# Kernel optimization log

Hardware: AMD Instinct MI355X
Metric: run time of the kernel (lower is better)

The kernel has to match this reference:

```python
import jax, jax.numpy as jnp
import numpy as np

B, S, D, H = 8, 1024, 768, 12
DH = D // H


def setup_inputs() -> dict:
    key = jax.random.key(0)
    ks = jax.random.split(key, 6)
    scale = 1.0 / np.sqrt(D)
    return {
        "inputs": jax.random.normal(ks[0], (B, S, D), dtype=jnp.float32),
        "Wq": jax.random.normal(ks[1], (D, D), dtype=jnp.float32) * scale,
        "bq": jnp.zeros((D,), jnp.float32),
        "Wk": jax.random.normal(ks[2], (D, D), dtype=jnp.float32) * scale,
        "bk": jnp.zeros((D,), jnp.float32),
        "Wv": jax.random.normal(ks[3], (D, D), dtype=jnp.float32) * scale,
        "bv": jnp.zeros((D,), jnp.float32),
        "Wo": jax.random.normal(ks[4], (D, D), dtype=jnp.float32) * scale,
        "bo": jnp.zeros((D,), jnp.float32),
    }


def _split_heads(x):
    # [B,S,D] -> [B,H,S,DH]
    b, s, _ = x.shape
    return x.reshape(b, s, H, DH).transpose(0, 2, 1, 3)


def reference(inputs, Wq, bq, Wk, bk, Wv, bv, Wo, bo):
    q = _split_heads(inputs @ Wq + bq)
    k = _split_heads(inputs @ Wk + bk)
    v = _split_heads(inputs @ Wv + bv)
    # scaled dot-product attention; scale = sqrt(projection_dim)
    scores = jnp.einsum("bhqd,bhkd->bhqk", q, k) / jnp.sqrt(jnp.float32(DH))
    weights = jax.nn.softmax(scores, axis=-1)
    attn = jnp.einsum("bhqk,bhkd->bhqd", weights, v)
    attn = attn.transpose(0, 2, 1, 3).reshape(inputs.shape[0], -1, D)
    return attn @ Wo + bo
```

## Files before the change

### kernel.cpp

```cpp
#include <hip/hip_runtime.h>
#include <math.h>

#define B 8
#define S 1024
#define D 768
#define H 12
#define DH 64
#define M_TOT (B * S)

typedef short bf16x8 __attribute__((ext_vector_type(8)));
typedef float f32x4 __attribute__((ext_vector_type(4)));

__device__ __forceinline__ unsigned short f2bf(float x) {
    unsigned u = __builtin_bit_cast(unsigned, x);
    u = (u + 0x7FFFu + ((u >> 16) & 1u)) >> 16;
    return (unsigned short)u;
}
__device__ __forceinline__ unsigned pk2bf(float a, float b) {
    return (unsigned)f2bf(a) | ((unsigned)f2bf(b) << 16);
}

__device__ __forceinline__ void async16(const unsigned short* g, unsigned short* l) {
    __builtin_amdgcn_global_load_lds((const __attribute__((address_space(1))) void*)g,
                                     (__attribute__((address_space(3))) void*)l, 16, 0, 0);
}

__device__ __forceinline__ void stage_tiles(const unsigned short* __restrict__ A,
                                            const unsigned short* __restrict__ Bt,
                                            unsigned short* At, unsigned short* Bs,
                                            int m0, int n0, int k0, int w, int srow, int scol) {
#pragma unroll
    for (int c = 0; c < 2; ++c) {
        const int cc = w * 2 + c;
        const int row = cc * 16 + srow;
        async16(&A[(size_t)(m0 + row) * D + k0 + scol], &At[cc * 512]);
        async16(&Bt[(size_t)(n0 + row) * D + k0 + scol], &Bs[cc * 512]);
    }
}

__global__ __launch_bounds__(256) void prep(const float* __restrict__ inputs,
                                            unsigned short* __restrict__ Abf,
                                            const float* W0, const float* W1,
                                            const float* W2, const float* W3,
                                            unsigned short* T0, unsigned short* T1,
                                            unsigned short* T2, unsigned short* T3) {
    const int bid = blockIdx.x;
    const int t = threadIdx.x;
    if (bid < 6144) {
        const int i = (bid * 256 + t) * 4;
        const float4 v = *(const float4*)&inputs[i];
        ushort4 o;
        o.x = f2bf(v.x); o.y = f2bf(v.y); o.z = f2bf(v.z); o.w = f2bf(v.w);
        *(ushort4*)&Abf[i] = o;
    } else {
        const int id = bid - 6144;
        const int z = id / 144;
        const int rem = id % 144;
        const int kx = rem % 12, ny = rem / 12;
        const float* Wsrc[4] = {W0, W1, W2, W3};
        unsigned short* Tdst[4] = {T0, T1, T2, T3};
        const float* Wm = Wsrc[z];
        unsigned short* Tm = Tdst[z];
        __shared__ float tile[64][65];
        const int r = t >> 4, c4 = (t & 15) * 4;
        const int k0 = kx * 64, n0 = ny * 64;
#pragma unroll
        for (int rr = 0; rr < 4; ++rr) {
            const float4 v = *(const float4*)&Wm[(size_t)(k0 + r + rr * 16) * D + n0 + c4];
            tile[r + rr * 16][c4 + 0] = v.x;
            tile[r + rr * 16][c4 + 1] = v.y;
            tile[r + rr * 16][c4 + 2] = v.z;
            tile[r + rr * 16][c4 + 3] = v.w;
        }
        __syncthreads();
#pragma unroll
        for (int rr = 0; rr < 4; ++rr) {
            const int nr = r + rr * 16;
            ushort4 o;
            o.x = f2bf(tile[c4 + 0][nr]);
            o.y = f2bf(tile[c4 + 1][nr]);
            o.z = f2bf(tile[c4 + 2][nr]);
            o.w = f2bf(tile[c4 + 3][nr]);
            *(ushort4*)&Tm[(size_t)(n0 + nr) * D + k0 + c4] = o;
        }
    }
}

__global__ __launch_bounds__(256) void gemm_qkv(const unsigned short* __restrict__ A,
                                                const unsigned short* __restrict__ Wtq,
                                                const unsigned short* __restrict__ Wtk,
                                                const unsigned short* __restrict__ Wtv,
                                                const float* __restrict__ bq,
                                                const float* __restrict__ bk,
                                                const float* __restrict__ bv,
                                                unsigned short* __restrict__ Qb,
                                                unsigned short* __restrict__ Kb,
                                                unsigned short* __restrict__ Vtb) {
    __shared__ unsigned short At[2][128 * 32];
    __shared__ unsigned short Bs[2][128 * 32];
    const int z = blockIdx.z;
    const unsigned short* Bt = (z == 0) ? Wtq : (z == 1) ? Wtk : Wtv;
    const float* bias = (z == 0) ? bq : (z == 1) ? bk : bv;
    const float scale = (z == 0) ? 0.125f : 1.0f;

    const int t = threadIdx.x;
    const int w = t >> 6, lane = t & 63;
    const int quad = lane >> 4, l15 = lane & 15;
    const int m0 = blockIdx.x * 128, n0 = blockIdx.y * 128;
    const int wm = (w & 1) * 64, wn = (w >> 1) * 64;
    const int srow = lane >> 2, scol = (lane & 3) * 8;

    f32x4 acc[4][4];
#pragma unroll
    for (int i = 0; i < 4; ++i)
#pragma unroll
        for (int j = 0; j < 4; ++j) acc[i][j] = (f32x4){0.f, 0.f, 0.f, 0.f};

    stage_tiles(A, Bt, At[0], Bs[0], m0, n0, 0, w, srow, scol);
    for (int kt = 0; kt < D / 32; ++kt) {
        unsigned short* Atc = At[kt & 1];
        unsigned short* Bsc = Bs[kt & 1];
        if (kt + 1 < D / 32) {
            stage_tiles(A, Bt, At[(kt + 1) & 1], Bs[(kt + 1) & 1], m0, n0, (kt + 1) * 32, w, srow, scol);
            __asm__ volatile("s_waitcnt vmcnt(4)" ::: "memory");
        } else {
            __asm__ volatile("s_waitcnt vmcnt(0)" ::: "memory");
        }
        __asm__ volatile("s_barrier" ::: "memory");
        bf16x8 af[4], bfr[4];
#pragma unroll
        for (int i = 0; i < 4; ++i)
            af[i] = *(const bf16x8*)&Atc[(wm + i * 16 + l15) * 32 + quad * 8];
#pragma unroll
        for (int j = 0; j < 4; ++j)
            bfr[j] = *(const bf16x8*)&Bsc[(wn + j * 16 + l15) * 32 + quad * 8];
#pragma unroll
        for (int i = 0; i < 4; ++i)
#pragma unroll
            for (int j = 0; j < 4; ++j)
                acc[i][j] = __builtin_amdgcn_mfma_f32_16x16x32_bf16(af[i], bfr[j], acc[i][j], 0, 0, 0);
        __asm__ volatile("s_barrier" ::: "memory");
    }

#pragma unroll
    for (int j = 0; j < 4; ++j) {
        const int col = n0 + wn + j * 16 + l15;
        const float bv2 = bias[col];
#pragma unroll
        for (int i = 0; i < 4; ++i) {
            const int row0 = m0 + wm + i * 16 + quad * 4;
            if (z < 2) {
                unsigned short* C = (z == 0) ? Qb : Kb;
#pragma unroll
                for (int r = 0; r < 4; ++r)
                    C[(size_t)(row0 + r) * D + col] = f2bf((acc[i][j][r] + bv2) * scale);
            } else {
                const int h = col >> 6, dh = col & 63;
                const int bb = row0 >> 10, s0 = row0 & 1023;
                ushort4 o;
                o.x = f2bf(acc[i][j][0] + bv2);
                o.y = f2bf(acc[i][j][1] + bv2);
                o.z = f2bf(acc[i][j][2] + bv2);
                o.w = f2bf(acc[i][j][3] + bv2);
                *(ushort4*)&Vtb[((size_t)(bb * H + h) * DH + dh) * S + s0] = o;
            }
        }
    }
}

__global__ __launch_bounds__(256) void gemm_out(const unsigned short* __restrict__ A,
                                                const unsigned short* __restrict__ Bt,
                                                const float* __restrict__ bias,
                                                float* __restrict__ C) {
    __shared__ unsigned short At[2][128 * 32];
    __shared__ unsigned short Bs[2][128 * 32];
    const int t = threadIdx.x;
    const int w = t >> 6, lane = t & 63;
    const int quad = lane >> 4, l15 = lane & 15;
    const int m0 = blockIdx.x * 128, n0 = blockIdx.y * 128;
    const int wm = (w & 1) * 64, wn = (w >> 1) * 64;
    const int srow = lane >> 2, scol = (lane & 3) * 8;

    f32x4 acc[4][4];
#pragma unroll
    for (int i = 0; i < 4; ++i)
#pragma unroll
        for (int j = 0; j < 4; ++j) acc[i][j] = (f32x4){0.f, 0.f, 0.f, 0.f};

    stage_tiles(A, Bt, At[0], Bs[0], m0, n0, 0, w, srow, scol);
    for (int kt = 0; kt < D / 32; ++kt) {
        unsigned short* Atc = At[kt & 1];
        unsigned short* Bsc = Bs[kt & 1];
        if (kt + 1 < D / 32) {
            stage_tiles(A, Bt, At[(kt + 1) & 1], Bs[(kt + 1) & 1], m0, n0, (kt + 1) * 32, w, srow, scol);
            __asm__ volatile("s_waitcnt vmcnt(4)" ::: "memory");
        } else {
            __asm__ volatile("s_waitcnt vmcnt(0)" ::: "memory");
        }
        __asm__ volatile("s_barrier" ::: "memory");
        bf16x8 af[4], bfr[4];
#pragma unroll
        for (int i = 0; i < 4; ++i)
            af[i] = *(const bf16x8*)&Atc[(wm + i * 16 + l15) * 32 + quad * 8];
#pragma unroll
        for (int j = 0; j < 4; ++j)
            bfr[j] = *(const bf16x8*)&Bsc[(wn + j * 16 + l15) * 32 + quad * 8];
#pragma unroll
        for (int i = 0; i < 4; ++i)
#pragma unroll
            for (int j = 0; j < 4; ++j)
                acc[i][j] = __builtin_amdgcn_mfma_f32_16x16x32_bf16(af[i], bfr[j], acc[i][j], 0, 0, 0);
        __asm__ volatile("s_barrier" ::: "memory");
    }

#pragma unroll
    for (int j = 0; j < 4; ++j) {
        const int col = n0 + wn + j * 16 + l15;
        const float bv = bias[col];
#pragma unroll
        for (int i = 0; i < 4; ++i) {
            const int row0 = m0 + wm + i * 16 + quad * 4;
#pragma unroll
            for (int r = 0; r < 4; ++r) C[(size_t)(row0 + r) * D + col] = acc[i][j][r] + bv;
        }
    }
}

__global__ __launch_bounds__(256) void attn_mfma(const unsigned short* __restrict__ Qg,
                                                 const unsigned short* __restrict__ Kg,
                                                 const unsigned short* __restrict__ Vtg,
                                                 unsigned short* __restrict__ ATT) {
    __shared__ unsigned short Ks[2 * 64 * 32];
    __shared__ unsigned short Vs[2 * 64 * 32];
    __shared__ unsigned short Ps2[4 * 32 * 72];

    const int t = threadIdx.x;
    const int w = t >> 6, lane = t & 63;
    const int quad = lane >> 4, l15 = lane & 15;
    const int bh = blockIdx.x % (B * H);
    const int q0 = (blockIdx.x / (B * H)) * 128;
    const int b = bh / H, h = bh % H;

    bf16x8 qb[2][2];
#pragma unroll
    for (int qh = 0; qh < 2; ++qh) {
        const size_t qoff = ((size_t)(b * S + q0 + w * 32 + qh * 16 + l15)) * D + h * DH;
        qb[qh][0] = *(const bf16x8*)&Qg[qoff + quad * 8];
        qb[qh][1] = *(const bf16x8*)&Qg[qoff + 32 + quad * 8];
    }

    f32x4 o[2][4];
#pragma unroll
    for (int qh = 0; qh < 2; ++qh)
#pragma unroll
        for (int n = 0; n < 4; ++n) o[qh][n] = (f32x4){0.f, 0.f, 0.f, 0.f};
    float m_r[2] = {-INFINITY, -INFINITY};
    float l_r[2] = {0.f, 0.f};

    const int srow = lane >> 2;
    const int scol = (((lane & 3) ^ ((lane >> 3) & 3))) * 8;
    const int fsw = ((quad ^ ((l15 >> 1) & 3)) * 8);

    unsigned short* myP = &Ps2[w * 32 * 72];

    for (int kt = 0; kt < S / 64; ++kt) {
        __syncthreads();
#pragma unroll
        for (int kc = 0; kc < 2; ++kc) {
            async16(&Kg[((size_t)(b * S + kt * 64 + w * 16 + srow)) * D + h * DH + kc * 32 + scol],
                    &Ks[kc * 2048 + w * 512]);
            async16(&Vtg[((size_t)(bh * DH + w * 16 + srow)) * S + kt * 64 + kc * 32 + scol],
                    &Vs[kc * 2048 + w * 512]);
        }
        __syncthreads();

        f32x4 sc[2][4];
#pragma unroll
        for (int n = 0; n < 4; ++n) {
            const bf16x8 ka0 = *(const bf16x8*)&Ks[0 * 2048 + (n * 16 + l15) * 32 + fsw];
            const bf16x8 ka1 = *(const bf16x8*)&Ks[1 * 2048 + (n * 16 + l15) * 32 + fsw];
#pragma unroll
            for (int qh = 0; qh < 2; ++qh) {
                f32x4 zz = (f32x4){0.f, 0.f, 0.f, 0.f};
                zz = __builtin_amdgcn_mfma_f32_16x16x32_bf16(ka0, qb[qh][0], zz, 0, 0, 0);
                zz = __builtin_amdgcn_mfma_f32_16x16x32_bf16(ka1, qb[qh][1], zz, 0, 0, 0);
                sc[qh][n] = zz;
            }
        }

        float alpha[2];
#pragma unroll
        for (int qh = 0; qh < 2; ++qh) {
            float rmax = -INFINITY;
#pragma unroll
            for (int n = 0; n < 4; ++n)
#pragma unroll
                for (int r = 0; r < 4; ++r) rmax = fmaxf(rmax, sc[qh][n][r]);
            rmax = fmaxf(rmax, __shfl_xor(rmax, 16, 64));
            rmax = fmaxf(rmax, __shfl_xor(rmax, 32, 64));
            const float mnew = fmaxf(m_r[qh], rmax);
            alpha[qh] = __expf(m_r[qh] - mnew);
            m_r[qh] = mnew;
            float rsum = 0.f;
#pragma unroll
            for (int n = 0; n < 4; ++n) {
                uint2 u;
                float p0 = __expf(sc[qh][n][0] - mnew);
                float p1 = __expf(sc[qh][n][1] - mnew);
                float p2 = __expf(sc[qh][n][2] - mnew);
                float p3 = __expf(sc[qh][n][3] - mnew);
                rsum += (p0 + p1) + (p2 + p3);
                u.x = pk2bf(p0, p1);
                u.y = pk2bf(p2, p3);
                *(uint2*)&myP[(qh * 16 + l15) * 72 + n * 16 + quad * 4] = u;
            }
            rsum += __shfl_xor(rsum, 16, 64);
            rsum += __shfl_xor(rsum, 32, 64);
            l_r[qh] = l_r[qh] * alpha[qh] + rsum;
#pragma unroll
            for (int n = 0; n < 4; ++n) o[qh][n] *= alpha[qh];
        }
        __asm__ volatile("s_waitcnt lgkmcnt(0)" ::: "memory");

        bf16x8 pb[2][2];
#pragma unroll
        for (int qh = 0; qh < 2; ++qh) {
            pb[qh][0] = *(const bf16x8*)&myP[(qh * 16 + l15) * 72 + 0 + quad * 8];
            pb[qh][1] = *(const bf16x8*)&myP[(qh * 16 + l15) * 72 + 32 + quad * 8];
        }

#pragma unroll
        for (int n = 0; n < 4; ++n) {
            const bf16x8 va0 = *(const bf16x8*)&Vs[0 * 2048 + (n * 16 + l15) * 32 + fsw];
            const bf16x8 va1 = *(const bf16x8*)&Vs[1 * 2048 + (n * 16 + l15) * 32 + fsw];
#pragma unroll
            for (int qh = 0; qh < 2; ++qh) {
                o[qh][n] = __builtin_amdgcn_mfma_f32_16x16x32_bf16(va0, pb[qh][0], o[qh][n], 0, 0, 0);
                o[qh][n] = __builtin_amdgcn_mfma_f32_16x16x32_bf16(va1, pb[qh][1], o[qh][n], 0, 0, 0);
            }
        }
    }

#pragma unroll
    for (int qh = 0; qh < 2; ++qh) {
        const float inv = 1.0f / l_r[qh];
        const size_t row = (size_t)(b * S + q0 + w * 32 + qh * 16 + l15) * D + h * DH;
#pragma unroll
        for (int n = 0; n < 4; ++n) {
            ushort4 ov;
            ov.x = f2bf(o[qh][n][0] * inv);
            ov.y = f2bf(o[qh][n][1] * inv);
            ov.z = f2bf(o[qh][n][2] * inv);
            ov.w = f2bf(o[qh][n][3] * inv);
            *(ushort4*)&ATT[row + n * 16 + quad * 4] = ov;
        }
    }
}

extern "C" void kernel_launch(void* const* d_in, const int* in_sizes, int n_in,
                              void* d_out, int out_size, void* d_ws, size_t ws_size,
                              hipStream_t stream) {
    const float* inputs = (const float*)d_in[0];
    const float* Wq = (const float*)d_in[1];
    const float* bq = (const float*)d_in[2];
    const float* Wk = (const float*)d_in[3];
    const float* bk = (const float*)d_in[4];
    const float* Wv = (const float*)d_in[5];
    const float* bv = (const float*)d_in[6];
    const float* Wo = (const float*)d_in[7];
    const float* bo = (const float*)d_in[8];

    const size_t nA = (size_t)M_TOT * D;
    unsigned short* Abf  = (unsigned short*)d_ws;
    unsigned short* Qb   = Abf + nA;
    unsigned short* Kb   = Qb + nA;
    unsigned short* Vtb  = Kb + nA;
    unsigned short* ATTb = Vtb + nA;
    unsigned short* Wtq  = ATTb + nA;
    unsigned short* Wtk  = Wtq + (size_t)D * D;
    unsigned short* Wtv  = Wtk + (size_t)D * D;
    unsigned short* Wto  = Wtv + (size_t)D * D;

    prep<<<6144 + 576, 256, 0, stream>>>(inputs, Abf, Wq, Wk, Wv, Wo, Wtq, Wtk, Wtv, Wto);

    gemm_qkv<<<dim3(M_TOT / 128, D / 128, 3), 256, 0, stream>>>(
        Abf, Wtq, Wtk, Wtv, bq, bk, bv, Qb, Kb, Vtb);

    attn_mfma<<<dim3((S / 128) * B * H), 256, 0, stream>>>(Qb, Kb, Vtb, ATTb);

    gemm_out<<<dim3(M_TOT / 128, D / 128), 256, 0, stream>>>(ATTb, Wto, bo, (float*)d_out);
}
```

Measured before the change: 222.4 us.

## Double-buffer K/V tiles in attention and use exp2 with folded log2e scale

The attention kernel now double-buffers the K and V tiles in LDS. It prefetches the next tile with async loads while computing on the current one, and uses vmcnt waits and raw barriers in place of two __syncthreads per iteration. The Q scale now folds in log2(e), so the softmax can call the hardware exp2 instruction directly. BF16 conversions switch to a cheaper round-half-up with a perm-based pack. This doubles the K/V LDS footprint, which may lower occupancy, and slightly changes rounding.

```diff
diff --git a/kernel.cpp b/kernel.cpp
--- a/kernel.cpp
+++ b/kernel.cpp
@@ -8,6 +8,8 @@
 #define DH 64
 #define M_TOT (B * S)
 
+#define QSCALE 0.18033688011112042f
+
 typedef short bf16x8 __attribute__((ext_vector_type(8)));
 typedef float f32x4 __attribute__((ext_vector_type(4)));
 
@@ -16,8 +18,13 @@
     u = (u + 0x7FFFu + ((u >> 16) & 1u)) >> 16;
     return (unsigned short)u;
 }
-__device__ __forceinline__ unsigned pk2bf(float a, float b) {
-    return (unsigned)f2bf(a) | ((unsigned)f2bf(b) << 16);
+__device__ __forceinline__ unsigned short f2bf_ru(float x) {
+    return (unsigned short)((__builtin_bit_cast(unsigned, x) + 0x8000u) >> 16);
+}
+__device__ __forceinline__ unsigned pk2bf_ru(float a, float b) {
+    unsigned ua = __builtin_bit_cast(unsigned, a) + 0x8000u;
+    unsigned ub = __builtin_bit_cast(unsigned, b) + 0x8000u;
+    return __builtin_amdgcn_perm(ub, ua, 0x07060302u);
 }
 
 __device__ __forceinline__ void async16(const unsigned short* g, unsigned short* l) {
@@ -101,7 +108,7 @@
     const int z = blockIdx.z;
     const unsigned short* Bt = (z == 0) ? Wtq : (z == 1) ? Wtk : Wtv;
     const float* bias = (z == 0) ? bq : (z == 1) ? bk : bv;
-    const float scale = (z == 0) ? 0.125f : 1.0f;
+    const float scale = (z == 0) ? QSCALE : 1.0f;
 
     const int t = threadIdx.x;
     const int w = t >> 6, lane = t & 63;
@@ -153,16 +160,14 @@
                 unsigned short* C = (z == 0) ? Qb : Kb;
 #pragma unroll
                 for (int r = 0; r < 4; ++r)
-                    C[(size_t)(row0 + r) * D + col] = f2bf((acc[i][j][r] + bv2) * scale);
+                    C[(size_t)(row0 + r) * D + col] = f2bf_ru((acc[i][j][r] + bv2) * scale);
             } else {
                 const int h = col >> 6, dh = col & 63;
                 const int bb = row0 >> 10, s0 = row0 & 1023;
-                ushort4 o;
-                o.x = f2bf(acc[i][j][0] + bv2);
-                o.y = f2bf(acc[i][j][1] + bv2);
-                o.z = f2bf(acc[i][j][2] + bv2);
-                o.w = f2bf(acc[i][j][3] + bv2);
-                *(ushort4*)&Vtb[((size_t)(bb * H + h) * DH + dh) * S + s0] = o;
+                uint2 u;
+                u.x = pk2bf_ru(acc[i][j][0] + bv2, acc[i][j][1] + bv2);
+                u.y = pk2bf_ru(acc[i][j][2] + bv2, acc[i][j][3] + bv2);
+                *(uint2*)&Vtb[((size_t)(bb * H + h) * DH + dh) * S + s0] = u;
             }
         }
     }
@@ -230,8 +235,8 @@
                                                  const unsigned short* __restrict__ Kg,
                                                  const unsigned short* __restrict__ Vtg,
                                                  unsigned short* __restrict__ ATT) {
-    __shared__ unsigned short Ks[2 * 64 * 32];
-    __shared__ unsigned short Vs[2 * 64 * 32];
+    __shared__ unsigned short Ks[2][2 * 64 * 32];
+    __shared__ unsigned short Vs[2][2 * 64 * 32];
     __shared__ unsigned short Ps2[4 * 32 * 72];
 
     const int t = threadIdx.x;
@@ -263,22 +268,34 @@
 
     unsigned short* myP = &Ps2[w * 32 * 72];
 
+    #define STAGE(ktv, bf)                                                                   \
+        {                                                                                     \
+            const int _kt = (ktv);                                                            \
+            _Pragma("unroll")                                                                 \
+            for (int kc = 0; kc < 2; ++kc) {                                                  \
+                async16(&Kg[((size_t)(b * S + _kt * 64 + w * 16 + srow)) * D + h * DH + kc * 32 + scol], \
+                        &Ks[bf][kc * 2048 + w * 512]);                                        \
+                async16(&Vtg[((size_t)(bh * DH + w * 16 + srow)) * S + _kt * 64 + kc * 32 + scol],       \
+                        &Vs[bf][kc * 2048 + w * 512]);                                        \
+            }                                                                                 \
+        }
+
+    STAGE(0, 0);
     for (int kt = 0; kt < S / 64; ++kt) {
-        __syncthreads();
-#pragma unroll
-        for (int kc = 0; kc < 2; ++kc) {
-            async16(&Kg[((size_t)(b * S + kt * 64 + w * 16 + srow)) * D + h * DH + kc * 32 + scol],
-                    &Ks[kc * 2048 + w * 512]);
-            async16(&Vtg[((size_t)(bh * DH + w * 16 + srow)) * S + kt * 64 + kc * 32 + scol],
-                    &Vs[kc * 2048 + w * 512]);
-        }
-        __syncthreads();
+        const int buf = kt & 1;
+        if (kt + 1 < S / 64) {
+            STAGE(kt + 1, buf ^ 1);
+            __asm__ volatile("s_waitcnt vmcnt(4)" ::: "memory");
+        } else {
+            __asm__ volatile("s_waitcnt vmcnt(0)" ::: "memory");
+        }
+        __asm__ volatile("s_barrier" ::: "memory");
 
         f32x4 sc[2][4];
 #pragma unroll
         for (int n = 0; n < 4; ++n) {
-            const bf16x8 ka0 = *(const bf16x8*)&Ks[0 * 2048 + (n * 16 + l15) * 32 + fsw];
-            const bf16x8 ka1 = *(const bf16x8*)&Ks[1 * 2048 + (n * 16 + l15) * 32 + fsw];
+            const bf16x8 ka0 = *(const bf16x8*)&Ks[buf][0 * 2048 + (n * 16 + l15) * 32 + fsw];
+            const bf16x8 ka1 = *(const bf16x8*)&Ks[buf][1 * 2048 + (n * 16 + l15) * 32 + fsw];
 #pragma unroll
             for (int qh = 0; qh < 2; ++qh) {
                 f32x4 zz = (f32x4){0.f, 0.f, 0.f, 0.f};
@@ -299,19 +316,19 @@
             rmax = fmaxf(rmax, __shfl_xor(rmax, 16, 64));
             rmax = fmaxf(rmax, __shfl_xor(rmax, 32, 64));
             const float mnew = fmaxf(m_r[qh], rmax);
-            alpha[qh] = __expf(m_r[qh] - mnew);
+            alpha[qh] = __builtin_amdgcn_exp2f(m_r[qh] - mnew);
             m_r[qh] = mnew;
             float rsum = 0.f;
 #pragma unroll
             for (int n = 0; n < 4; ++n) {
+                const float p0 = __builtin_amdgcn_exp2f(sc[qh][n][0] - mnew);
+                const float p1 = __builtin_amdgcn_exp2f(sc[qh][n][1] - mnew);
+                const float p2 = __builtin_amdgcn_exp2f(sc[qh][n][2] - mnew);
+                const float p3 = __builtin_amdgcn_exp2f(sc[qh][n][3] - mnew);
+                rsum += (p0 + p1) + (p2 + p3);
                 uint2 u;
-                float p0 = __expf(sc[qh][n][0] - mnew);
-                float p1 = __expf(sc[qh][n][1] - mnew);
-                float p2 = __expf(sc[qh][n][2] - mnew);
-                float p3 = __expf(sc[qh][n][3] - mnew);
-                rsum += (p0 + p1) + (p2 + p3);
-                u.x = pk2bf(p0, p1);
-                u.y = pk2bf(p2, p3);
+                u.x = pk2bf_ru(p0, p1);
+                u.y = pk2bf_ru(p2, p3);
                 *(uint2*)&myP[(qh * 16 + l15) * 72 + n * 16 + quad * 4] = u;
             }
             rsum += __shfl_xor(rsum, 16, 64);
@@ -331,15 +348,17 @@
 
 #pragma unroll
         for (int n = 0; n < 4; ++n) {
-            const bf16x8 va0 = *(const bf16x8*)&Vs[0 * 2048 + (n * 16 + l15) * 32 + fsw];
-            const bf16x8 va1 = *(const bf16x8*)&Vs[1 * 2048 + (n * 16 + l15) * 32 + fsw];
+            const bf16x8 va0 = *(const bf16x8*)&Vs[buf][0 * 2048 + (n * 16 + l15) * 32 + fsw];
+            const bf16x8 va1 = *(const bf16x8*)&Vs[buf][1 * 2048 + (n * 16 + l15) * 32 + fsw];
 #pragma unroll
             for (int qh = 0; qh < 2; ++qh) {
                 o[qh][n] = __builtin_amdgcn_mfma_f32_16x16x32_bf16(va0, pb[qh][0], o[qh][n], 0, 0, 0);
                 o[qh][n] = __builtin_amdgcn_mfma_f32_16x16x32_bf16(va1, pb[qh][1], o[qh][n], 0, 0, 0);
             }
         }
-    }
+        __asm__ volatile("s_barrier" ::: "memory");
+    }
+    #undef STAGE
 
 #pragma unroll
     for (int qh = 0; qh < 2; ++qh) {
@@ -347,12 +366,10 @@
         const size_t row = (size_t)(b * S + q0 + w * 32 + qh * 16 + l15) * D + h * DH;
 #pragma unroll
         for (int n = 0; n < 4; ++n) {
-            ushort4 ov;
-            ov.x = f2bf(o[qh][n][0] * inv);
-            ov.y = f2bf(o[qh][n][1] * inv);
-            ov.z = f2bf(o[qh][n][2] * inv);
-            ov.w = f2bf(o[qh][n][3] * inv);
-            *(ushort4*)&ATT[row + n * 16 + quad * 4] = ov;
+            uint2 u;
+            u.x = pk2bf_ru(o[qh][n][0] * inv, o[qh][n][1] * inv);
+            u.y = pk2bf_ru(o[qh][n][2] * inv, o[qh][n][3] * inv);
+            *(uint2*)&ATT[row + n * 16 + quad * 4] = u;
         }
     }
 }
```

Result: faster. 215.4 us (-3.1%).
